# Performance work log

Hardware: AMD Instinct MI355X
Metric: run time of the kernel (lower is better)

Reference implementation:

```python
import jax, jax.numpy as jnp
import numpy as np

N_NODES = 131072
N_EDGES = 2097152
IN_DIM = 768
HID = 64
NODES_PER_GRAPH = 32
OUT_DIM = 2


def setup_inputs() -> dict:
    key = jax.random.key(0)
    k1, k2, k3, k4 = jax.random.split(key, 4)
    x = jax.random.normal(k1, (N_NODES, IN_DIM), dtype=jnp.float32)
    edge_index = jax.random.randint(k2, (2, N_EDGES), 0, N_NODES, dtype=jnp.int64)
    W_conv = jax.random.normal(k3, (IN_DIM, HID), dtype=jnp.float32) * 0.02
    b_conv = jnp.zeros((HID,), dtype=jnp.float32)
    W_lin = jax.random.normal(k4, (OUT_DIM, HID * NODES_PER_GRAPH), dtype=jnp.float32) * 0.02
    b_lin = jnp.zeros((OUT_DIM,), dtype=jnp.float32)
    return {"x": x, "edge_index": edge_index, "W_conv": W_conv,
            "b_conv": b_conv, "W_lin": W_lin, "b_lin": b_lin}


def reference(x, edge_index, W_conv, b_conv, W_lin, b_lin):
    N = x.shape[0]
    # GCNConv: add self-loops, symmetric normalization D^-1/2 (A+I) D^-1/2
    loops = jnp.arange(N, dtype=edge_index.dtype)
    src = jnp.concatenate([edge_index[0], loops])  # [E+N]
    dst = jnp.concatenate([edge_index[1], loops])
    deg = jax.ops.segment_sum(jnp.ones_like(dst, dtype=x.dtype), dst, num_segments=N)
    dinv = jax.lax.rsqrt(deg)  # deg >= 1 due to self-loops
    norm = dinv[src] * dinv[dst]  # [E+N]
    h = x @ W_conv  # [N, HID]
    msg = h[src] * norm[:, None]  # gather + scale
    out = jax.ops.segment_sum(msg, dst, num_segments=N) + b_conv  # scatter-add
    out = jax.nn.relu(out)
    out = out.reshape(-1, HID * NODES_PER_GRAPH)  # [B, 2048]
    logits = out @ W_lin.T + b_lin  # [B, OUT_DIM]
    return jax.nn.log_softmax(logits, axis=1)
```

## Files before the change

kernel.cpp:

```cpp
#include <hip/hip_runtime.h>
#include <hip/hip_bf16.h>

#define N_NODES 131072
#define N_EDGES 2097152
#define IN_DIM 768
#define HID 64
#define NPG 32
#define NGRAPH (N_NODES / NPG)

#define BM 128
#define GEMM_BLOCKS (N_NODES / BM)

#define RNG 128
#define NB (N_NODES / RNG)
#define EPB 4096
#define NCB (N_EDGES / EPB)
#define PBLK 8
#define RPB (NCB / PBLK)
#define PREP_BLK 192

typedef __attribute__((ext_vector_type(8))) short bf16x8;
typedef __attribute__((ext_vector_type(4))) float f32x4;

static __device__ __forceinline__ unsigned short f2bf(float f) {
    __hip_bfloat16 h = __float2bfloat16(f);
    return *reinterpret_cast<unsigned short*>(&h);
}
static __device__ __forceinline__ float bf2f(unsigned short s) {
    return __uint_as_float(((unsigned int)s) << 16);
}

__global__ __launch_bounds__(256) void gcn_prep_count(const float* __restrict__ W,
                                                      unsigned short* __restrict__ Wt,
                                                      const int* __restrict__ dst,
                                                      unsigned int* __restrict__ C) {
    __shared__ unsigned int hist[NB];
    int tid = threadIdx.x;
    if (blockIdx.x < PREP_BLK) {
        int i = blockIdx.x * 256 + tid;
        if (i < IN_DIM * HID) {
            int k = i >> 6, n = i & 63;
            Wt[n * IN_DIM + k] = f2bf(W[i]);
        }
        return;
    }
    int cb = blockIdx.x - PREP_BLK;
    for (int t = tid; t < NB; t += 256) hist[t] = 0u;
    __syncthreads();
    int base = cb * EPB;
    #pragma unroll
    for (int u = 0; u < EPB / 256; ++u) {
        int d = dst[base + u * 256 + tid];
        atomicAdd(&hist[d >> 7], 1u);
    }
    __syncthreads();
    for (int t = tid; t < NB; t += 256) C[(size_t)cb * NB + t] = hist[t];
}

__global__ __launch_bounds__(256) void gcn_prefA(unsigned int* __restrict__ C,
                                                 unsigned int* __restrict__ S) {
    int tid = threadIdx.x;
    int p = blockIdx.x;
    #pragma unroll
    for (int c = 0; c < 4; ++c) {
        int t = tid + c * 256;
        unsigned int run = 0;
        for (int r = 0; r < RPB; r += 8) {
            unsigned int v[8];
            size_t base = ((size_t)(p * RPB + r)) * NB + t;
            #pragma unroll
            for (int j = 0; j < 8; ++j) v[j] = C[base + (size_t)j * NB];
            #pragma unroll
            for (int j = 0; j < 8; ++j) { C[base + (size_t)j * NB] = run; run += v[j]; }
        }
        S[p * NB + t] = run;
    }
}

__global__ __launch_bounds__(256) void gcn_prefB(unsigned int* __restrict__ S,
                                                 unsigned int* __restrict__ bstart) {
    __shared__ unsigned int sm[256];
    int tid = threadIdx.x;
    unsigned int lexcl[4];
    unsigned int lrun = 0;
    #pragma unroll
    for (int j = 0; j < 4; ++j) {
        unsigned int t = tid * 4 + j;
        unsigned int r = 0;
        #pragma unroll
        for (int p = 0; p < PBLK; ++p) {
            unsigned int v = S[p * NB + t];
            S[p * NB + t] = r;
            r += v;
        }
        lexcl[j] = lrun;
        lrun += r;
    }
    sm[tid] = lrun;
    __syncthreads();
    for (int off = 1; off < 256; off <<= 1) {
        unsigned int u = (tid >= off) ? sm[tid - off] : 0u;
        __syncthreads();
        sm[tid] += u;
        __syncthreads();
    }
    unsigned int texcl = sm[tid] - lrun;
    #pragma unroll
    for (int j = 0; j < 4; ++j) bstart[tid * 4 + j] = texcl + lexcl[j];
    if (tid == 255) bstart[NB] = N_EDGES;
}

__global__ __launch_bounds__(256) void gcn_scatter(const int* __restrict__ src,
                                                   const int* __restrict__ dst,
                                                   const unsigned int* __restrict__ C,
                                                   const unsigned int* __restrict__ S,
                                                   const unsigned int* __restrict__ bstart,
                                                   unsigned int* __restrict__ part) {
    __shared__ unsigned int off[NB];
    int tid = threadIdx.x, cb = blockIdx.x;
    int p = cb >> 6;
    for (int t = tid; t < NB; t += 256)
        off[t] = bstart[t] + S[p * NB + t] + C[(size_t)cb * NB + t];
    __syncthreads();
    int base = cb * EPB;
    #pragma unroll
    for (int u = 0; u < EPB / 256; ++u) {
        int i = base + u * 256 + tid;
        int d = dst[i];
        unsigned int pos = atomicAdd(&off[d >> 7], 1u);
        part[pos] = (unsigned int)src[i] | ((unsigned int)(d & (RNG - 1)) << 17);
    }
}

__global__ __launch_bounds__(256) void gcn_sort2(const unsigned int* __restrict__ part,
                                                 const unsigned int* __restrict__ bstart,
                                                 unsigned int* __restrict__ part2,
                                                 unsigned int* __restrict__ nstart,
                                                 float* __restrict__ dinv) {
    __shared__ unsigned int hist[RNG];
    __shared__ unsigned int sc[RNG];
    __shared__ unsigned int off[RNG];
    int tid = threadIdx.x, b = blockIdx.x;
    if (tid < RNG) hist[tid] = 0u;
    __syncthreads();
    unsigned int s0 = bstart[b], s1 = bstart[b + 1];
    for (unsigned int j = s0 + tid; j < s1; j += 256)
        atomicAdd(&hist[part[j] >> 17], 1u);
    __syncthreads();
    if (tid < RNG) sc[tid] = hist[tid];
    __syncthreads();
    #pragma unroll
    for (int o = 1; o < RNG; o <<= 1) {
        unsigned int u = (tid < RNG && tid >= o) ? sc[tid - o] : 0u;
        __syncthreads();
        if (tid < RNG) sc[tid] += u;
        __syncthreads();
    }
    if (tid < RNG) {
        unsigned int excl = sc[tid] - hist[tid];
        nstart[b * RNG + tid] = s0 + excl;
        off[tid] = s0 + excl;
        dinv[b * RNG + tid] = rsqrtf((float)(hist[tid] + 1));
    }
    if (b == NB - 1 && tid == 0) nstart[N_NODES] = N_EDGES;
    __syncthreads();
    for (unsigned int j = s0 + tid; j < s1; j += 256) {
        unsigned int pr = part[j];
        unsigned int pos = atomicAdd(&off[pr >> 17], 1u);
        part2[pos] = pr & 0x1FFFF;
    }
}

__global__ __launch_bounds__(256) void gcn_gemm(const float* __restrict__ x,
                                                const unsigned short* __restrict__ Wt,
                                                const float* __restrict__ dinv,
                                                unsigned short* __restrict__ hsb) {
    int tid = threadIdx.x;
    int lane = tid & 63;
    int w = tid >> 6;
    int rowbase = blockIdx.x * BM;
    int rl = lane & 15;
    int kq = (lane >> 4) * 8;

    const float* xa0 = x + (size_t)(rowbase + w * 32 + rl) * IN_DIM + kq;
    const float* xa1 = xa0 + (size_t)16 * IN_DIM;
    const unsigned short* wp = Wt + (size_t)rl * IN_DIM + kq;

    f32x4 acc[2][4] = {};

    #pragma unroll 2
    for (int kb = 0; kb < IN_DIM; kb += 32) {
        float4 u0 = *(const float4*)(xa0 + kb);
        float4 u1 = *(const float4*)(xa0 + kb + 4);
        float4 u2 = *(const float4*)(xa1 + kb);
        float4 u3 = *(const float4*)(xa1 + kb + 4);
        bf16x8 b0 = *(const bf16x8*)(wp + kb);
        bf16x8 b1 = *(const bf16x8*)(wp + (size_t)16 * IN_DIM + kb);
        bf16x8 b2 = *(const bf16x8*)(wp + (size_t)32 * IN_DIM + kb);
        bf16x8 b3 = *(const bf16x8*)(wp + (size_t)48 * IN_DIM + kb);
        bf16x8 a0, a1;
        a0[0] = (short)f2bf(u0.x); a0[1] = (short)f2bf(u0.y);
        a0[2] = (short)f2bf(u0.z); a0[3] = (short)f2bf(u0.w);
        a0[4] = (short)f2bf(u1.x); a0[5] = (short)f2bf(u1.y);
        a0[6] = (short)f2bf(u1.z); a0[7] = (short)f2bf(u1.w);
        a1[0] = (short)f2bf(u2.x); a1[1] = (short)f2bf(u2.y);
        a1[2] = (short)f2bf(u2.z); a1[3] = (short)f2bf(u2.w);
        a1[4] = (short)f2bf(u3.x); a1[5] = (short)f2bf(u3.y);
        a1[6] = (short)f2bf(u3.z); a1[7] = (short)f2bf(u3.w);
        acc[0][0] = __builtin_amdgcn_mfma_f32_16x16x32_bf16(a0, b0, acc[0][0], 0, 0, 0);
        acc[1][0] = __builtin_amdgcn_mfma_f32_16x16x32_bf16(a1, b0, acc[1][0], 0, 0, 0);
        acc[0][1] = __builtin_amdgcn_mfma_f32_16x16x32_bf16(a0, b1, acc[0][1], 0, 0, 0);
        acc[1][1] = __builtin_amdgcn_mfma_f32_16x16x32_bf16(a1, b1, acc[1][1], 0, 0, 0);
        acc[0][2] = __builtin_amdgcn_mfma_f32_16x16x32_bf16(a0, b2, acc[0][2], 0, 0, 0);
        acc[1][2] = __builtin_amdgcn_mfma_f32_16x16x32_bf16(a1, b2, acc[1][2], 0, 0, 0);
        acc[0][3] = __builtin_amdgcn_mfma_f32_16x16x32_bf16(a0, b3, acc[0][3], 0, 0, 0);
        acc[1][3] = __builtin_amdgcn_mfma_f32_16x16x32_bf16(a1, b3, acc[1][3], 0, 0, 0);
    }
    #pragma unroll
    for (int rt = 0; rt < 2; ++rt) {
        int row0 = rowbase + w * 32 + rt * 16 + (lane >> 4) * 4;
        #pragma unroll
        for (int rr = 0; rr < 4; ++rr) {
            float dv = dinv[row0 + rr];
            #pragma unroll
            for (int ct = 0; ct < 4; ++ct) {
                int col = ct * 16 + rl;
                hsb[(size_t)(row0 + rr) * HID + col] = f2bf(acc[rt][ct][rr] * dv);
            }
        }
    }
}

__global__ __launch_bounds__(512) void gcn_agg(const unsigned short* __restrict__ hsb,
                                               const unsigned int* __restrict__ part2,
                                               const unsigned int* __restrict__ nstart,
                                               const float* __restrict__ dinv,
                                               const float* __restrict__ b_conv,
                                               const float* __restrict__ W_lin,
                                               const float* __restrict__ b_lin,
                                               float* __restrict__ out) {
    __shared__ float p0s[8], p1s[8];
    int tid = threadIdx.x, lane = tid & 63, w = tid >> 6;
    int g = blockIdx.x;
    float bc = b_conv[lane];
    float l0 = 0.f, l1 = 0.f;

    int i0 = g * NPG + w * 4;
    int cc[4];
    unsigned int stt[4];
    float dii[4];
    int sidx[4];
    float av[4];
    #pragma unroll
    for (int k = 0; k < 4; ++k) {
        int i = i0 + k;
        unsigned int st = nstart[i], en = nstart[i + 1];
        stt[k] = st;
        cc[k] = (int)(en - st);
        dii[k] = dinv[i];
    }
    #pragma unroll
    for (int k = 0; k < 4; ++k)
        sidx[k] = (lane < cc[k]) ? (int)part2[stt[k] + lane] : (i0 + k);
    #pragma unroll
    for (int k = 0; k < 4; ++k)
        av[k] = bf2f(hsb[(size_t)(i0 + k) * HID + lane]);

    int cmax = max(max(cc[0], cc[1]), max(cc[2], cc[3]));
    int clim = min(cmax, 64);
    for (int e = 0; e < clim; e += 4) {
        float v[4][4];
        #pragma unroll
        for (int k = 0; k < 4; ++k) {
            #pragma unroll
            for (int j = 0; j < 4; ++j) {
                int idx = e + j;
                int cl = idx < cc[k] ? idx : 0;
                int s = __shfl(sidx[k], cl);
                v[k][j] = bf2f(hsb[(size_t)s * HID + lane]);
            }
        }
        #pragma unroll
        for (int k = 0; k < 4; ++k) {
            #pragma unroll
            for (int j = 0; j < 4; ++j)
                if (e + j < cc[k]) av[k] += v[k][j];
        }
    }
    #pragma unroll
    for (int k = 0; k < 4; ++k)
        for (int e2 = 64; e2 < cc[k]; ++e2)
            av[k] += bf2f(hsb[(size_t)part2[stt[k] + e2] * HID + lane]);

    #pragma unroll
    for (int k = 0; k < 4; ++k) {
        int node = w * 4 + k;
        float v = fmaxf(fmaf(av[k], dii[k], bc), 0.f);
        l0 = fmaf(v, W_lin[node * HID + lane], l0);
        l1 = fmaf(v, W_lin[HID * NPG + node * HID + lane], l1);
    }
    #pragma unroll
    for (int d = 32; d > 0; d >>= 1) {
        l0 += __shfl_down(l0, d);
        l1 += __shfl_down(l1, d);
    }
    if (lane == 0) { p0s[w] = l0; p1s[w] = l1; }
    __syncthreads();
    if (tid == 0) {
        float A = b_lin[0], B = b_lin[1];
        #pragma unroll
        for (int j = 0; j < 8; ++j) { A += p0s[j]; B += p1s[j]; }
        float m = fmaxf(A, B);
        float lse = m + logf(expf(A - m) + expf(B - m));
        out[g * 2 + 0] = A - lse;
        out[g * 2 + 1] = B - lse;
    }
}

extern "C" void kernel_launch(void* const* d_in, const int* in_sizes, int n_in,
                              void* d_out, int out_size, void* d_ws, size_t ws_size,
                              hipStream_t stream) {
    const float* x  = (const float*)d_in[0];
    const int* ei   = (const int*)d_in[1];
    const float* Wc = (const float*)d_in[2];
    const float* bc = (const float*)d_in[3];
    const float* Wl = (const float*)d_in[4];
    const float* bl = (const float*)d_in[5];
    float* out = (float*)d_out;

    char* ws = (char*)d_ws;
    unsigned short* Wt   = (unsigned short*)(ws);
    float*          dinv = (float*)(ws + (128 << 10));
    unsigned int*  bstart= (unsigned int*)(ws + (640 << 10));
    unsigned int*  S     = (unsigned int*)(ws + (656 << 10));
    unsigned int*  part2 = (unsigned int*)(ws + (1u << 20));
    unsigned int*  nstart= (unsigned int*)(ws + (9u << 20));
    unsigned int*  C     = (unsigned int*)(ws + (10u << 20));
    unsigned int*  part  = (unsigned int*)(ws + (12u << 20));
    unsigned short* hsb  = (unsigned short*)(ws + (10u << 20));

    const int* srcIdx = ei;
    const int* dstIdx = ei + N_EDGES;

    gcn_prep_count<<<PREP_BLK + NCB, 256, 0, stream>>>(Wc, Wt, dstIdx, C);
    gcn_prefA<<<PBLK, 256, 0, stream>>>(C, S);
    gcn_prefB<<<1, 256, 0, stream>>>(S, bstart);
    gcn_scatter<<<NCB, 256, 0, stream>>>(srcIdx, dstIdx, C, S, bstart, part);
    gcn_sort2<<<NB, 256, 0, stream>>>(part, bstart, part2, nstart, dinv);
    gcn_gemm<<<GEMM_BLOCKS, 256, 0, stream>>>(x, Wt, dinv, hsb);
    gcn_agg<<<NGRAPH, 512, 0, stream>>>(hsb, part2, nstart, dinv, bc, Wl, bl, out);
}
```

Measured before the change: 248.5 us.

## Fuse prefix/scatter/sort/GEMM into persistent cooperative kernel overlapping GEMM with CSR build

Merges the prefix-sum, scatter, second-level sort and GEMM kernels into one cooperative persistent kernel. Blocks 512-767 start pulling GEMM tiles from an atomic queue straight away, while blocks 0-511 build the CSR through flag-based global barriers and then join the GEMM queue. To drop the GEMM's dependency on dinv, the source-side degree scaling moves into the aggregation kernel, which now loads and shuffles per-edge dinv. The aim is to cut launch gaps and hide the sort phases behind the x-reading GEMM, at the cost of spin-wait barriers, extra dinv gathers in aggregation, and a fallback path of separate launches.

Result: slower. 557.1 us (+124.1%).

```diff
diff --git a/kernel.cpp b/kernel.cpp
--- a/kernel.cpp
+++ b/kernel.cpp
@@ -10,6 +10,7 @@
 
 #define BM 128
 #define GEMM_BLOCKS (N_NODES / BM)
+#define MEGA_BLOCKS 768
 
 #define RNG 128
 #define NB (N_NODES / RNG)
@@ -30,37 +31,8 @@
     return __uint_as_float(((unsigned int)s) << 16);
 }
 
-__global__ __launch_bounds__(256) void gcn_prep_count(const float* __restrict__ W,
-                                                      unsigned short* __restrict__ Wt,
-                                                      const int* __restrict__ dst,
-                                                      unsigned int* __restrict__ C) {
-    __shared__ unsigned int hist[NB];
-    int tid = threadIdx.x;
-    if (blockIdx.x < PREP_BLK) {
-        int i = blockIdx.x * 256 + tid;
-        if (i < IN_DIM * HID) {
-            int k = i >> 6, n = i & 63;
-            Wt[n * IN_DIM + k] = f2bf(W[i]);
-        }
-        return;
-    }
-    int cb = blockIdx.x - PREP_BLK;
-    for (int t = tid; t < NB; t += 256) hist[t] = 0u;
-    __syncthreads();
-    int base = cb * EPB;
-    #pragma unroll
-    for (int u = 0; u < EPB / 256; ++u) {
-        int d = dst[base + u * 256 + tid];
-        atomicAdd(&hist[d >> 7], 1u);
-    }
-    __syncthreads();
-    for (int t = tid; t < NB; t += 256) C[(size_t)cb * NB + t] = hist[t];
-}
-
-__global__ __launch_bounds__(256) void gcn_prefA(unsigned int* __restrict__ C,
-                                                 unsigned int* __restrict__ S) {
-    int tid = threadIdx.x;
-    int p = blockIdx.x;
+static __device__ __forceinline__ void dev_prefA(int p, unsigned int* C, unsigned int* S) {
+    int tid = threadIdx.x;
     #pragma unroll
     for (int c = 0; c < 4; ++c) {
         int t = tid + c * 256;
@@ -77,9 +49,8 @@
     }
 }
 
-__global__ __launch_bounds__(256) void gcn_prefB(unsigned int* __restrict__ S,
-                                                 unsigned int* __restrict__ bstart) {
-    __shared__ unsigned int sm[256];
+static __device__ __forceinline__ void dev_prefB(unsigned int* S, unsigned int* bstart,
+                                                 unsigned int* sm) {
     int tid = threadIdx.x;
     unsigned int lexcl[4];
     unsigned int lrun = 0;
@@ -110,14 +81,11 @@
     if (tid == 255) bstart[NB] = N_EDGES;
 }
 
-__global__ __launch_bounds__(256) void gcn_scatter(const int* __restrict__ src,
-                                                   const int* __restrict__ dst,
-                                                   const unsigned int* __restrict__ C,
-                                                   const unsigned int* __restrict__ S,
-                                                   const unsigned int* __restrict__ bstart,
-                                                   unsigned int* __restrict__ part) {
-    __shared__ unsigned int off[NB];
-    int tid = threadIdx.x, cb = blockIdx.x;
+static __device__ __forceinline__ void dev_scatter(int cb, const int* src, const int* dst,
+                                                   const unsigned int* C, const unsigned int* S,
+                                                   const unsigned int* bstart,
+                                                   unsigned int* part, unsigned int* off) {
+    int tid = threadIdx.x;
     int p = cb >> 6;
     for (int t = tid; t < NB; t += 256)
         off[t] = bstart[t] + S[p * NB + t] + C[(size_t)cb * NB + t];
@@ -132,15 +100,14 @@
     }
 }
 
-__global__ __launch_bounds__(256) void gcn_sort2(const unsigned int* __restrict__ part,
-                                                 const unsigned int* __restrict__ bstart,
-                                                 unsigned int* __restrict__ part2,
-                                                 unsigned int* __restrict__ nstart,
-                                                 float* __restrict__ dinv) {
-    __shared__ unsigned int hist[RNG];
-    __shared__ unsigned int sc[RNG];
-    __shared__ unsigned int off[RNG];
-    int tid = threadIdx.x, b = blockIdx.x;
+static __device__ __forceinline__ void dev_sort2(int b, const unsigned int* part,
+                                                 const unsigned int* bstart,
+                                                 unsigned int* part2, unsigned int* nstart,
+                                                 float* dinv, unsigned int* sm) {
+    unsigned int* hist = sm;
+    unsigned int* sc   = sm + RNG;
+    unsigned int* off  = sm + 2 * RNG;
+    int tid = threadIdx.x;
     if (tid < RNG) hist[tid] = 0u;
     __syncthreads();
     unsigned int s0 = bstart[b], s1 = bstart[b + 1];
@@ -171,14 +138,13 @@
     }
 }
 
-__global__ __launch_bounds__(256) void gcn_gemm(const float* __restrict__ x,
-                                                const unsigned short* __restrict__ Wt,
-                                                const float* __restrict__ dinv,
-                                                unsigned short* __restrict__ hsb) {
+static __device__ __forceinline__ void dev_gemm_tile(int gb, const float* x,
+                                                     const unsigned short* Wt,
+                                                     unsigned short* hsb) {
     int tid = threadIdx.x;
     int lane = tid & 63;
     int w = tid >> 6;
-    int rowbase = blockIdx.x * BM;
+    int rowbase = gb * BM;
     int rl = lane & 15;
     int kq = (lane >> 4) * 8;
 
@@ -220,15 +186,139 @@
     for (int rt = 0; rt < 2; ++rt) {
         int row0 = rowbase + w * 32 + rt * 16 + (lane >> 4) * 4;
         #pragma unroll
-        for (int rr = 0; rr < 4; ++rr) {
-            float dv = dinv[row0 + rr];
+        for (int ct = 0; ct < 4; ++ct)
             #pragma unroll
-            for (int ct = 0; ct < 4; ++ct) {
+            for (int rr = 0; rr < 4; ++rr) {
                 int col = ct * 16 + rl;
-                hsb[(size_t)(row0 + rr) * HID + col] = f2bf(acc[rt][ct][rr] * dv);
+                hsb[(size_t)(row0 + rr) * HID + col] = f2bf(acc[rt][ct][rr]);
             }
-        }
-    }
+    }
+}
+
+__global__ __launch_bounds__(256) void gcn_prep_count(const float* __restrict__ W,
+                                                      unsigned short* __restrict__ Wt,
+                                                      const int* __restrict__ dst,
+                                                      unsigned int* __restrict__ C,
+                                                      unsigned int* __restrict__ flags) {
+    __shared__ unsigned int hist[NB];
+    int tid = threadIdx.x;
+    if (blockIdx.x == 0 && tid < 8) flags[tid] = 0u;
+    if (blockIdx.x < PREP_BLK) {
+        int i = blockIdx.x * 256 + tid;
+        if (i < IN_DIM * HID) {
+            int k = i >> 6, n = i & 63;
+            Wt[n * IN_DIM + k] = f2bf(W[i]);
+        }
+        return;
+    }
+    int cb = blockIdx.x - PREP_BLK;
+    for (int t = tid; t < NB; t += 256) hist[t] = 0u;
+    __syncthreads();
+    int base = cb * EPB;
+    #pragma unroll
+    for (int u = 0; u < EPB / 256; ++u) {
+        int d = dst[base + u * 256 + tid];
+        atomicAdd(&hist[d >> 7], 1u);
+    }
+    __syncthreads();
+    for (int t = tid; t < NB; t += 256) C[(size_t)cb * NB + t] = hist[t];
+}
+
+static __device__ __forceinline__ void waitCnt(unsigned int* f, unsigned int target) {
+    if (threadIdx.x == 0) {
+        while (__hip_atomic_load(f, __ATOMIC_RELAXED, __HIP_MEMORY_SCOPE_AGENT) < target)
+            __builtin_amdgcn_s_sleep(16);
+    }
+    __syncthreads();
+    __threadfence();
+}
+
+__global__ __launch_bounds__(256, 3) void gcn_mega(const float* __restrict__ x,
+                                                   const unsigned short* __restrict__ Wt,
+                                                   unsigned short* __restrict__ hsb,
+                                                   const int* __restrict__ src,
+                                                   const int* __restrict__ dst,
+                                                   unsigned int* __restrict__ C,
+                                                   unsigned int* __restrict__ S,
+                                                   unsigned int* __restrict__ bstart,
+                                                   unsigned int* __restrict__ part,
+                                                   unsigned int* __restrict__ part2,
+                                                   unsigned int* __restrict__ nstart,
+                                                   float* __restrict__ dinv,
+                                                   unsigned int* __restrict__ flags) {
+    __shared__ unsigned int smem[NB];
+    __shared__ int tileS;
+    int b = blockIdx.x, tid = threadIdx.x;
+    unsigned int* fA = flags + 0;
+    unsigned int* fB = flags + 1;
+    unsigned int* fS = flags + 2;
+    unsigned int* qc = flags + 3;
+
+    if (b < 512) {
+        if (b < PBLK) {
+            dev_prefA(b, C, S);
+            __syncthreads();
+            __threadfence();
+            if (tid == 0) atomicAdd(fA, 1u);
+        }
+        if (b == 0) {
+            waitCnt(fA, PBLK);
+            dev_prefB(S, bstart, smem);
+            __syncthreads();
+            __threadfence();
+            if (tid == 0) atomicExch(fB, 1u);
+        }
+        waitCnt(fB, 1u);
+        dev_scatter(b, src, dst, C, S, bstart, part, smem);
+        __syncthreads();
+        __threadfence();
+        if (tid == 0) atomicAdd(fS, 1u);
+        waitCnt(fS, 512u);
+        dev_sort2(b, part, bstart, part2, nstart, dinv, smem);
+        __syncthreads();
+        dev_sort2(b + 512, part, bstart, part2, nstart, dinv, smem);
+        __syncthreads();
+    }
+    for (;;) {
+        __syncthreads();
+        if (tid == 0) tileS = (int)atomicAdd(qc, 1u);
+        __syncthreads();
+        int t = tileS;
+        if (t >= GEMM_BLOCKS) break;
+        dev_gemm_tile(t, x, Wt, hsb);
+    }
+}
+
+__global__ __launch_bounds__(256) void gcn_prefA_k(unsigned int* __restrict__ C,
+                                                   unsigned int* __restrict__ S) {
+    dev_prefA(blockIdx.x, C, S);
+}
+__global__ __launch_bounds__(256) void gcn_prefB_k(unsigned int* __restrict__ S,
+                                                   unsigned int* __restrict__ bstart) {
+    __shared__ unsigned int sm[256];
+    dev_prefB(S, bstart, sm);
+}
+__global__ __launch_bounds__(256) void gcn_scatter_k(const int* __restrict__ src,
+                                                     const int* __restrict__ dst,
+                                                     const unsigned int* __restrict__ C,
+                                                     const unsigned int* __restrict__ S,
+                                                     const unsigned int* __restrict__ bstart,
+                                                     unsigned int* __restrict__ part) {
+    __shared__ unsigned int off[NB];
+    dev_scatter(blockIdx.x, src, dst, C, S, bstart, part, off);
+}
+__global__ __launch_bounds__(256) void gcn_sort2_k(const unsigned int* __restrict__ part,
+                                                   const unsigned int* __restrict__ bstart,
+                                                   unsigned int* __restrict__ part2,
+                                                   unsigned int* __restrict__ nstart,
+                                                   float* __restrict__ dinv) {
+    __shared__ unsigned int sm[3 * RNG];
+    dev_sort2(blockIdx.x, part, bstart, part2, nstart, dinv, sm);
+}
+__global__ __launch_bounds__(256) void gcn_gemm_k(const float* __restrict__ x,
+                                                  const unsigned short* __restrict__ Wt,
+                                                  unsigned short* __restrict__ hsb) {
+    dev_gemm_tile(blockIdx.x, x, Wt, hsb);
 }
 
 __global__ __launch_bounds__(512) void gcn_agg(const unsigned short* __restrict__ hsb,
@@ -250,6 +340,7 @@
     unsigned int stt[4];
     float dii[4];
     int sidx[4];
+    float dsv[4];
     float av[4];
     #pragma unroll
     for (int k = 0; k < 4; ++k) {
@@ -260,11 +351,13 @@
         dii[k] = dinv[i];
     }
     #pragma unroll
+    for (int k = 0; k < 4; ++k) {
+        sidx[k] = (lane < cc[k]) ? (int)part2[stt[k] + lane] : (i0 + k);
+        dsv[k] = (lane < cc[k]) ? dinv[sidx[k]] : 0.f;
+    }
+    #pragma unroll
     for (int k = 0; k < 4; ++k)
-        sidx[k] = (lane < cc[k]) ? (int)part2[stt[k] + lane] : (i0 + k);
-    #pragma unroll
-    for (int k = 0; k < 4; ++k)
-        av[k] = bf2f(hsb[(size_t)(i0 + k) * HID + lane]);
+        av[k] = dii[k] * bf2f(hsb[(size_t)(i0 + k) * HID + lane]);
 
     int cmax = max(max(cc[0], cc[1]), max(cc[2], cc[3]));
     int clim = min(cmax, 64);
@@ -277,7 +370,8 @@
                 int idx = e + j;
                 int cl = idx < cc[k] ? idx : 0;
                 int s = __shfl(sidx[k], cl);
-                v[k][j] = bf2f(hsb[(size_t)s * HID + lane]);
+                float ds = __shfl(dsv[k], cl);
+                v[k][j] = ds * bf2f(hsb[(size_t)s * HID + lane]);
             }
         }
         #pragma unroll
@@ -289,8 +383,10 @@
     }
     #pragma unroll
     for (int k = 0; k < 4; ++k)
-        for (int e2 = 64; e2 < cc[k]; ++e2)
-            av[k] += bf2f(hsb[(size_t)part2[stt[k] + e2] * HID + lane]);
+        for (int e2 = 64; e2 < cc[k]; ++e2) {
+            int s = (int)part2[stt[k] + e2];
+            av[k] += dinv[s] * bf2f(hsb[(size_t)s * HID + lane]);
+        }
 
     #pragma unroll
     for (int k = 0; k < 4; ++k) {
@@ -329,24 +425,34 @@
     float* out = (float*)d_out;
 
     char* ws = (char*)d_ws;
-    unsigned short* Wt   = (unsigned short*)(ws);
-    float*          dinv = (float*)(ws + (128 << 10));
-    unsigned int*  bstart= (unsigned int*)(ws + (640 << 10));
-    unsigned int*  S     = (unsigned int*)(ws + (656 << 10));
-    unsigned int*  part2 = (unsigned int*)(ws + (1u << 20));
-    unsigned int*  nstart= (unsigned int*)(ws + (9u << 20));
-    unsigned int*  C     = (unsigned int*)(ws + (10u << 20));
-    unsigned int*  part  = (unsigned int*)(ws + (12u << 20));
-    unsigned short* hsb  = (unsigned short*)(ws + (10u << 20));
+    unsigned short* Wt    = (unsigned short*)(ws);
+    float*          dinv  = (float*)(ws + (128 << 10));
+    unsigned int*  bstart = (unsigned int*)(ws + (640 << 10));
+    unsigned int*  S      = (unsigned int*)(ws + (656 << 10));
+    unsigned int*  flags  = (unsigned int*)(ws + (768 << 10));
+    unsigned int*  part2  = (unsigned int*)(ws + (1u << 20));
+    unsigned int*  nstart = (unsigned int*)(ws + (9u << 20));
+    unsigned int*  C      = (unsigned int*)(ws + (10u << 20));
+    unsigned int*  part   = (unsigned int*)(ws + (12u << 20));
+    unsigned short* hsb   = (unsigned short*)(ws + (20u << 20));
 
     const int* srcIdx = ei;
     const int* dstIdx = ei + N_EDGES;
 
-    gcn_prep_count<<<PREP_BLK + NCB, 256, 0, stream>>>(Wc, Wt, dstIdx, C);
-    gcn_prefA<<<PBLK, 256, 0, stream>>>(C, S);
-    gcn_prefB<<<1, 256, 0, stream>>>(S, bstart);
-    gcn_scatter<<<NCB, 256, 0, stream>>>(srcIdx, dstIdx, C, S, bstart, part);
-    gcn_sort2<<<NB, 256, 0, stream>>>(part, bstart, part2, nstart, dinv);
-    gcn_gemm<<<GEMM_BLOCKS, 256, 0, stream>>>(x, Wt, dinv, hsb);
+    gcn_prep_count<<<PREP_BLK + NCB, 256, 0, stream>>>(Wc, Wt, dstIdx, C, flags);
+
+    void* margs[] = { (void*)&x, (void*)&Wt, (void*)&hsb, (void*)&srcIdx, (void*)&dstIdx,
+                      (void*)&C, (void*)&S, (void*)&bstart, (void*)&part, (void*)&part2,
+                      (void*)&nstart, (void*)&dinv, (void*)&flags };
+    hipError_t err = hipLaunchCooperativeKernel((void*)gcn_mega, dim3(MEGA_BLOCKS),
+                                                dim3(256), margs, 0, stream);
+    if (err != hipSuccess) {
+        gcn_prefA_k<<<PBLK, 256, 0, stream>>>(C, S);
+        gcn_prefB_k<<<1, 256, 0, stream>>>(S, bstart);
+        gcn_scatter_k<<<NCB, 256, 0, stream>>>(srcIdx, dstIdx, C, S, bstart, part);
+        gcn_sort2_k<<<NB, 256, 0, stream>>>(part, bstart, part2, nstart, dinv);
+        gcn_gemm_k<<<GEMM_BLOCKS, 256, 0, stream>>>(x, Wt, hsb);
+    }
+
     gcn_agg<<<NGRAPH, 512, 0, stream>>>(hsb, part2, nstart, dinv, bc, Wl, bl, out);
 }
```
